# Performance work log

Hardware: AMD Instinct MI355X
Metric: run time of the kernel (lower is better)

The kernel has to match this reference:

```python
import jax, jax.numpy as jnp
import numpy as np

C = 1024  # channel dim
T = 2048  # max context / actual seq len
B = 8

def setup_inputs() -> dict:
    key = jax.random.key(0)
    k1, k2, k3 = jax.random.split(key, 3)
    x = jax.random.normal(k1, (B, T, C), dtype=jnp.float32)
    # torch nn.Linear(C, 3C, bias=False): y = x @ W.T, W shape [3C, C].
    # We store the pre-transposed [C, 3C] / [C, C] matrices for clean matmuls.
    scale = 1.0 / np.sqrt(C)
    Wqkv = jax.random.normal(k2, (C, 3 * C), dtype=jnp.float32) * scale
    Wproj = jax.random.normal(k3, (C, C), dtype=jnp.float32) * scale
    return {"x": x, "Wqkv": Wqkv, "Wproj": Wproj}

def reference(x, Wqkv, Wproj):
    t = x.shape[1]
    qkv = x @ Wqkv                      # [B, t, 3C]
    q, k, v = jnp.split(qkv, 3, axis=-1)  # each [B, t, C]
    w = jnp.einsum('btc,bsc->bts', q, k) * (C ** -0.5)  # [B, t, t]
    causal = jnp.triu(jnp.ones((t, t), dtype=bool), k=1)
    w = jnp.where(causal, -jnp.inf, w)
    a = jax.nn.softmax(w, axis=-1)      # [B, t, t]
    out = jnp.einsum('bts,bsc->btc', a, v)  # [B, t, C]
    return out @ Wproj
```

## Files before the change

kernel.cpp:

```cpp
#include <hip/hip_runtime.h>

typedef unsigned short u16;
typedef __attribute__((ext_vector_type(8))) short bf16x8;
typedef __attribute__((ext_vector_type(4))) float f32x4;

__device__ __forceinline__ u16 f2bf(float f) {
    unsigned u = __float_as_uint(f);
    u += 0x7fffu + ((u >> 16) & 1u);
    return (u16)(u >> 16);
}

__device__ __forceinline__ void g2l16(const void* g, void* l) {
    __builtin_amdgcn_global_load_lds((const __attribute__((address_space(1))) void*)g,
                                     (__attribute__((address_space(3))) void*)l, 16, 0, 0);
}

#define SPACK_ELEMS 2228224LL

#define BM 128
#define BN 128
#define BK 64

template <bool OUT_BF16>
__global__ __launch_bounds__(256, 4) void gemm_bt(
    const u16* __restrict__ A, const u16* __restrict__ B, void* __restrict__ Cout,
    int K, int lda, int ldb, int ldc,
    long long sA, long long sB, long long sC,
    float alpha, int mode)
{
    int bx, by;
    int bz = blockIdx.z;
    if (mode == 1) {
        int l;
        if (gridDim.z == 8) {
            int g = (int)blockIdx.x + (int)gridDim.x * (int)blockIdx.z;
            bz = g & 7; l = g >> 3;
        } else {
            l = blockIdx.x;
        }
        by = (int)((sqrtf(8.f * (float)l + 1.f) - 1.f) * 0.5f);
        while ((by + 1) * (by + 2) / 2 <= l) ++by;
        while (by * (by + 1) / 2 > l) --by;
        bx = l - by * (by + 1) / 2;
    } else if (mode == 2) {
        if (gridDim.z == 8) {
            int g = (int)blockIdx.x
                  + (int)gridDim.x * ((int)blockIdx.y
                  + (int)gridDim.y * (int)blockIdx.z);
            bz = g & 7;
            int h = g >> 3;
            int a  = h >> 5;
            int qp = (h >> 2) & 7;
            int rr = h & 3;
            const int MS[4][4] = {{15, 2, 1,12},
                                  { 4, 9,10, 7},
                                  { 8, 5, 6,11},
                                  { 3,14,13, 0}};
            bx = qp;
            by = MS[(a + qp) & 3][rr];
        } else {
            bx = blockIdx.x;
            int byrev = ((int)blockIdx.y + 4 * ((int)blockIdx.z >> 1)) & 15;
            by = (int)gridDim.y - 1 - byrev;
        }
    } else {
        bx = blockIdx.x; by = blockIdx.y;
    }
    int Keff = K;
    if (mode == 2) { int cap = (by + 1) * BM; if (cap < Keff) Keff = cap; }

    __shared__ alignas(16) u16 As[BM * BK];
    __shared__ alignas(16) u16 Bs[BN * BK];

    const int tid  = threadIdx.x;
    const int wave = tid >> 6, lane = tid & 63;
    const int wm = wave >> 1, wn = wave & 1;
    const int q = lane >> 4, r = lane & 15;

    const long long Pby = 16384LL * (by * (by + 1) / 2);

    const u16* Ab;
    int lda_e = lda;
    if (mode == 2) {
        lda_e = 2 * (by + 1) * BM;
        Ab = A + sA * bz + 2 * Pby;
    } else {
        Ab = A + sA * bz + (size_t)(by * BM) * lda_e;
    }
    const u16* Bb = B + sB * bz + (size_t)(bx * BN) * ldb;

    const u16* ap[4]; const u16* bp[4]; int sb[4];
#pragma unroll
    for (int j = 0; j < 4; ++j) {
        int s   = (wave * 4 + j) * 64 + lane;
        int row = s >> 3;
        int cc  = (s & 7) ^ (row & 7);
        ap[j] = Ab + (size_t)row * lda_e + cc * 8;
        bp[j] = Bb + (size_t)row * ldb + cc * 8;
        sb[j] = (wave * 4 + j) * 64;
    }

    f32x4 acc[4][4] = {};

    const int kiters = Keff / BK;
    for (int kt = 0; kt < kiters; ++kt) {
#pragma unroll
        for (int j = 0; j < 4; ++j) { g2l16(ap[j], As + (size_t)sb[j] * 8); ap[j] += BK; }
#pragma unroll
        for (int j = 0; j < 4; ++j) { g2l16(bp[j], Bs + (size_t)sb[j] * 8); bp[j] += BK; }
        __syncthreads();
#pragma unroll
        for (int ks = 0; ks < 2; ++ks) {
            bf16x8 af[4], bfv[4];
#pragma unroll
            for (int i = 0; i < 4; ++i) {
                int mr = wm * 64 + i * 16 + r;
                int cc = (ks * 4 + q) ^ (mr & 7);
                af[i] = *(const bf16x8*)(As + mr * BK + cc * 8);
            }
#pragma unroll
            for (int i = 0; i < 4; ++i) {
                int nr = wn * 64 + i * 16 + r;
                int cc = (ks * 4 + q) ^ (nr & 7);
                bfv[i] = *(const bf16x8*)(Bs + nr * BK + cc * 8);
            }
#pragma unroll
            for (int i = 0; i < 4; ++i)
#pragma unroll
                for (int jn = 0; jn < 4; ++jn)
                    acc[i][jn] = __builtin_amdgcn_mfma_f32_16x16x32_bf16(
                        af[i], bfv[jn], acc[i][jn], 0, 0, 0);
        }
        __syncthreads();
    }

    if (mode == 1) {
        float* Cp = (float*)Cout + sC * bz + Pby;
        const int ldrow = (by + 1) * BM;
#pragma unroll
        for (int i = 0; i < 4; ++i) {
            int lr = wm * 64 + i * 16 + q * 4;
#pragma unroll
            for (int jn = 0; jn < 4; ++jn) {
                int col = bx * BN + wn * 64 + jn * 16 + r;
#pragma unroll
                for (int rr = 0; rr < 4; ++rr)
                    Cp[(size_t)(lr + rr) * ldrow + col] = acc[i][jn][rr] * alpha;
            }
        }
    } else if constexpr (OUT_BF16) {
        u16* Cp = (u16*)Cout + sC * bz;
#pragma unroll
        for (int i = 0; i < 4; ++i) {
            int rowb = by * BM + wm * 64 + i * 16 + q * 4;
#pragma unroll
            for (int jn = 0; jn < 4; ++jn) {
                int col = bx * BN + wn * 64 + jn * 16 + r;
#pragma unroll
                for (int rr = 0; rr < 4; ++rr)
                    Cp[(size_t)(rowb + rr) * ldc + col] = f2bf(acc[i][jn][rr] * alpha);
            }
        }
    } else {
        float* Cp = (float*)Cout + sC * bz;
#pragma unroll
        for (int i = 0; i < 4; ++i) {
            int rowb = by * BM + wm * 64 + i * 16 + q * 4;
#pragma unroll
            for (int jn = 0; jn < 4; ++jn) {
                int col = bx * BN + wn * 64 + jn * 16 + r;
#pragma unroll
                for (int rr = 0; rr < 4; ++rr)
                    Cp[(size_t)(rowb + rr) * ldc + col] = acc[i][jn][rr] * alpha;
            }
        }
    }
}

__global__ void cast_f32_bf16(const float4* __restrict__ in, ushort4* __restrict__ out) {
    int i = blockIdx.x * 256 + threadIdx.x;
    float4 f = in[i];
    ushort4 o;
    o.x = f2bf(f.x); o.y = f2bf(f.y); o.z = f2bf(f.z); o.w = f2bf(f.w);
    out[i] = o;
}

__global__ void transpose_cast_f32(const float* __restrict__ in, u16* __restrict__ out,
                                   int R, int Cc) {
    __shared__ u16 tile[32][33];
    int tx = threadIdx.x, ty = threadIdx.y;
    int c0 = blockIdx.x * 32, r0 = blockIdx.y * 32;
#pragma unroll
    for (int k = 0; k < 4; ++k)
        tile[ty + k * 8][tx] = f2bf(in[(size_t)(r0 + ty + k * 8) * Cc + c0 + tx]);
    __syncthreads();
#pragma unroll
    for (int k = 0; k < 4; ++k)
        out[(size_t)(c0 + ty + k * 8) * R + r0 + tx] = tile[tx][ty + k * 8];
}

__global__ __launch_bounds__(256) void softmax_causal_packed(
    float* __restrict__ S, long long sS)
{
    const int wave = threadIdx.x >> 6, lane = threadIdx.x & 63;
    int zb, xb;
    if (gridDim.y == 8) {
        int g = (int)blockIdx.x + (int)gridDim.x * (int)blockIdx.y;
        zb = g & 7; xb = g >> 3;
    } else {
        zb = blockIdx.y; xb = blockIdx.x;
    }
    const int t = xb * 4 + wave;
    const int by = t >> 7, lr = t & 127;
    const int L = (by + 1) << 7;
    float* row = S + (long long)zb * sS
               + 16384LL * (by * (by + 1) / 2) + (size_t)lr * L;
    const int n = t + 1;
    const int nit = (L + 255) >> 8;

    float v[32];
    float m = -1e30f;
    for (int it = 0; it < nit; ++it) {
        int c = it * 64 + lane;
        int e = c * 4;
        float4 f = make_float4(-1e30f, -1e30f, -1e30f, -1e30f);
        if (e < n) f = ((const float4*)row)[c];
        v[it * 4 + 0] = (e + 0 < n) ? f.x : -1e30f;
        v[it * 4 + 1] = (e + 1 < n) ? f.y : -1e30f;
        v[it * 4 + 2] = (e + 2 < n) ? f.z : -1e30f;
        v[it * 4 + 3] = (e + 3 < n) ? f.w : -1e30f;
        m = fmaxf(m, fmaxf(fmaxf(v[it * 4 + 0], v[it * 4 + 1]),
                           fmaxf(v[it * 4 + 2], v[it * 4 + 3])));
    }
    for (int off = 32; off > 0; off >>= 1) m = fmaxf(m, __shfl_xor(m, off));

    float s = 0.f;
    for (int it = 0; it < nit; ++it) {
#pragma unroll
        for (int j = 0; j < 4; ++j) {
            v[it * 4 + j] = __expf(v[it * 4 + j] - m);
            s += v[it * 4 + j];
        }
    }
    for (int off = 32; off > 0; off >>= 1) s += __shfl_xor(s, off);
    float inv = 1.f / s;

    u16* orow = (u16*)row;
    for (int it = 0; it < nit; ++it) {
        int c = it * 64 + lane;
        if (c * 4 < L) {
            ushort4 o;
            o.x = f2bf(v[it * 4 + 0] * inv);
            o.y = f2bf(v[it * 4 + 1] * inv);
            o.z = f2bf(v[it * 4 + 2] * inv);
            o.w = f2bf(v[it * 4 + 3] * inv);
            ((ushort4*)orow)[c] = o;
        }
    }
}

extern "C" void kernel_launch(void* const* d_in, const int* in_sizes, int n_in,
                              void* d_out, int out_size, void* d_ws, size_t ws_size,
                              hipStream_t stream)
{
    const float* x     = (const float*)d_in[0];
    const float* Wqkv  = (const float*)d_in[1];
    const float* Wproj = (const float*)d_in[2];
    float* out = (float*)d_out;

    const int Bb = 8, T = 2048, C1 = 1024, C3 = 3072;

    char* ws = (char*)d_ws;
    u16*  xb     = (u16*)(ws);
    u16*  VWpT   = (u16*)(ws);
    u16*  WqkvT  = (u16*)(ws +  33554432ULL);
    u16*  WprojT = (u16*)(ws +  39845888ULL);
    u16*  qkvb   = (u16*)(ws +  41943040ULL);
    float* Sbuf  = (float*)(ws + 142606336ULL);

    const unsigned long long sbytes = SPACK_ELEMS * 4ULL;
    int zc = 1;
    if      (ws_size >= 142606336ULL + 8ULL * sbytes) zc = 8;
    else if (ws_size >= 142606336ULL + 4ULL * sbytes) zc = 4;
    else if (ws_size >= 142606336ULL + 2ULL * sbytes) zc = 2;

    cast_f32_bf16<<<16384, 256, 0, stream>>>((const float4*)x, (ushort4*)xb);

    transpose_cast_f32<<<dim3(96, 32), dim3(32, 8), 0, stream>>>(Wqkv,  WqkvT,  C1, C3);
    transpose_cast_f32<<<dim3(32, 32), dim3(32, 8), 0, stream>>>(Wproj, WprojT, C1, C1);

    gemm_bt<true><<<dim3(24, 128, 1), 256, 0, stream>>>(
        xb, WqkvT, qkvb, C1, C1, C1, C3, 0, 0, 0, 1.0f, 0);

    gemm_bt<true><<<dim3(16, 8, 8), 256, 0, stream>>>(
        WprojT, qkvb + 2 * C1, VWpT, C1, C1, C3, T,
        0, (long long)T * C3, (long long)C1 * T, 1.0f, 0);

    for (int i = 0; i < Bb; i += zc) {
        const u16* qb   = qkvb + (long long)i * T * C3;
        const u16* kb   = qb + C1;
        const u16* vwpb = VWpT + (long long)i * C1 * T;
        float* ob = out + (long long)i * T * C1;

        gemm_bt<false><<<dim3(136, 1, zc), 256, 0, stream>>>(
            qb, kb, Sbuf, C1, C3, C3, 0,
            (long long)T * C3, (long long)T * C3, SPACK_ELEMS,
            0.03125f, 1);

        softmax_causal_packed<<<dim3(T / 4, zc), 256, 0, stream>>>(
            Sbuf, SPACK_ELEMS);

        gemm_bt<false><<<dim3(8, 16, zc), 256, 0, stream>>>(
            (const u16*)Sbuf, vwpb, ob, T, 0, T, C1,
            2LL * SPACK_ELEMS, (long long)C1 * T, (long long)T * C1,
            1.0f, 2);
    }

    (void)in_sizes; (void)n_in; (void)out_size;
}
```

Before: 382.0 us.

## Fuse input cast and weight transposes into one kernel, simplify mode-2 tile mapping

Merges the x bf16 cast and the two weight transpose-cast kernels into a single launch that dispatches on block index, removing two kernel launches and their gaps. Also replaces the magic-square tile assignment in the causal PV GEMM mode with a plain row-major (bx = h&7, by = h>>3) mapping. The simpler mapping drops the load balancing of triangular work across consecutively scheduled blocks, so heavy tiles may cluster and cause tail imbalance.

Result: no change. 386.4 us (+1.2%).

```diff
diff --git a/kernel.cpp b/kernel.cpp
--- a/kernel.cpp
+++ b/kernel.cpp
@@ -49,15 +49,8 @@
                   + (int)gridDim.y * (int)blockIdx.z);
             bz = g & 7;
             int h = g >> 3;
-            int a  = h >> 5;
-            int qp = (h >> 2) & 7;
-            int rr = h & 3;
-            const int MS[4][4] = {{15, 2, 1,12},
-                                  { 4, 9,10, 7},
-                                  { 8, 5, 6,11},
-                                  { 3,14,13, 0}};
-            bx = qp;
-            by = MS[(a + qp) & 3][rr];
+            bx = h & 7;
+            by = h >> 3;
         } else {
             bx = blockIdx.x;
             int byrev = ((int)blockIdx.y + 4 * ((int)blockIdx.z >> 1)) & 15;
@@ -177,19 +170,32 @@
     }
 }
 
-__global__ void cast_f32_bf16(const float4* __restrict__ in, ushort4* __restrict__ out) {
-    int i = blockIdx.x * 256 + threadIdx.x;
-    float4 f = in[i];
-    ushort4 o;
-    o.x = f2bf(f.x); o.y = f2bf(f.y); o.z = f2bf(f.z); o.w = f2bf(f.w);
-    out[i] = o;
-}
-
-__global__ void transpose_cast_f32(const float* __restrict__ in, u16* __restrict__ out,
-                                   int R, int Cc) {
+__global__ __launch_bounds__(256) void pre_cast_all(
+    const float* __restrict__ x,     u16* __restrict__ xb,
+    const float* __restrict__ Wqkv,  u16* __restrict__ WqkvT,
+    const float* __restrict__ Wproj, u16* __restrict__ WprojT)
+{
     __shared__ u16 tile[32][33];
-    int tx = threadIdx.x, ty = threadIdx.y;
-    int c0 = blockIdx.x * 32, r0 = blockIdx.y * 32;
+    const int b = blockIdx.x;
+    if (b < 16384) {
+        int i = b * 256 + threadIdx.x;
+        float4 f = ((const float4*)x)[i];
+        ushort4 o;
+        o.x = f2bf(f.x); o.y = f2bf(f.y); o.z = f2bf(f.z); o.w = f2bf(f.w);
+        ((ushort4*)xb)[i] = o;
+        return;
+    }
+    const float* in; u16* out; int R, Cc, c0, r0;
+    if (b < 16384 + 3072) {
+        int l = b - 16384;
+        in = Wqkv; out = WqkvT; R = 1024; Cc = 3072;
+        c0 = (l % 96) * 32; r0 = (l / 96) * 32;
+    } else {
+        int l = b - 16384 - 3072;
+        in = Wproj; out = WprojT; R = 1024; Cc = 1024;
+        c0 = (l % 32) * 32; r0 = (l / 32) * 32;
+    }
+    const int tx = threadIdx.x & 31, ty = threadIdx.x >> 5;
 #pragma unroll
     for (int k = 0; k < 4; ++k)
         tile[ty + k * 8][tx] = f2bf(in[(size_t)(r0 + ty + k * 8) * Cc + c0 + tx]);
@@ -284,10 +290,8 @@
     else if (ws_size >= 142606336ULL + 4ULL * sbytes) zc = 4;
     else if (ws_size >= 142606336ULL + 2ULL * sbytes) zc = 2;
 
-    cast_f32_bf16<<<16384, 256, 0, stream>>>((const float4*)x, (ushort4*)xb);
-
-    transpose_cast_f32<<<dim3(96, 32), dim3(32, 8), 0, stream>>>(Wqkv,  WqkvT,  C1, C3);
-    transpose_cast_f32<<<dim3(32, 32), dim3(32, 8), 0, stream>>>(Wproj, WprojT, C1, C1);
+    pre_cast_all<<<16384 + 3072 + 1024, 256, 0, stream>>>(
+        x, xb, Wqkv, WqkvT, Wproj, WprojT);
 
     gemm_bt<true><<<dim3(24, 128, 1), 256, 0, stream>>>(
         xb, WqkvT, qkvb, C1, C1, C1, C3, 0, 0, 0, 1.0f, 0);
```
